# Kernel optimization log

Hardware: AMD Instinct MI355X
Metric: run time of the kernel (lower is better)

The kernel has to match this reference:

```python
import jax, jax.numpy as jnp
import numpy as np

OMEGA = 1.5

def _sine(x, W, b, omega=OMEGA):
    return jnp.sin(omega * (x @ W.T + b))

def setup_inputs() -> dict:
    key = jax.random.key(0)
    ks = jax.random.split(key, 17)
    I = J = K = 384
    mid, R = 256, 100
    s = 0.05  # small init scale, mimics uniform(-1/in, 1/in) style init
    return {
        "A_input": jax.random.normal(ks[0], (I, 1), jnp.float32),
        "B_input": jax.random.normal(ks[1], (J, 1), jnp.float32),
        "C_input": jax.random.normal(ks[2], (K, 1), jnp.float32),
        "A_W1": jax.random.normal(ks[3], (mid, 1), jnp.float32) * s,
        "A_b1": jax.random.normal(ks[4], (mid,), jnp.float32) * s,
        "A_W2": jax.random.normal(ks[5], (R, mid), jnp.float32) * s,
        "A_b2": jax.random.normal(ks[6], (R,), jnp.float32) * s,
        "B_W1": jax.random.normal(ks[7], (mid, 1), jnp.float32) * s,
        "B_b1": jax.random.normal(ks[8], (mid,), jnp.float32) * s,
        "B_W2": jax.random.normal(ks[9], (R, mid), jnp.float32) * s,
        "B_b2": jax.random.normal(ks[10], (R,), jnp.float32) * s,
        "C_W1": jax.random.normal(ks[11], (mid, 1), jnp.float32) * s,
        "C_b1": jax.random.normal(ks[12], (mid,), jnp.float32) * s,
        "C_W2": jax.random.normal(ks[13], (mid, mid), jnp.float32) * s,
        "C_b2": jax.random.normal(ks[14], (mid,), jnp.float32) * s,
        "C_W3": jax.random.normal(ks[15], (R, mid), jnp.float32) * s,
        "C_b3": jax.random.normal(ks[16], (R,), jnp.float32) * s,
    }

def reference(A_input, B_input, C_input,
              A_W1, A_b1, A_W2, A_b2,
              B_W1, B_b1, B_W2, B_b2,
              C_W1, C_b1, C_W2, C_b2, C_W3, C_b3):
    # Factor networks
    A = _sine(A_input, A_W1, A_b1) @ A_W2.T + A_b2                  # [I, R]
    B = _sine(B_input, B_W1, B_b1) @ B_W2.T + B_b2                  # [J, R]
    C = _sine(_sine(C_input, C_W1, C_b1), C_W2, C_b2) @ C_W3.T + C_b3  # [K, R]
    # The frozen core is super-diagonal (core[r,r,r]=1), so the permute/matmul
    # chain reduces exactly to the CP contraction sum_r A[i,r]*B[j,r]*C[k,r].
    return jnp.einsum('ir,jr,kr->ijk', A, B, C)  # [I, J, K]
```

## Files before the change

kernel.cpp:

```cpp
#include <hip/hip_runtime.h>
#include <hip/hip_bf16.h>

#define RR 100
#define MID 256
#define NN 384
#define KP 128

typedef __attribute__((ext_vector_type(8))) __bf16 bf16x8;
typedef __attribute__((ext_vector_type(4))) float floatx4;
typedef unsigned short ushort_t;

#define SW(row, ch) ((((row) << 7)) + ((((ch) ^ ((row) & 15))) << 3))

__device__ __forceinline__ ushort_t f2bf(float f) {
  __hip_bfloat16 h = __float2bfloat16(f);
  return __builtin_bit_cast(ushort_t, h);
}

__global__ __launch_bounds__(256) void factors_kernel(
    const float* __restrict__ xA, const float* __restrict__ xB,
    const float* __restrict__ xC,
    const float* __restrict__ AW1, const float* __restrict__ Ab1,
    const float* __restrict__ AW2, const float* __restrict__ Ab2,
    const float* __restrict__ BW1, const float* __restrict__ Bb1,
    const float* __restrict__ BW2, const float* __restrict__ Bb2,
    const float* __restrict__ CW1, const float* __restrict__ Cb1,
    const float* __restrict__ CW2, const float* __restrict__ Cb2,
    const float* __restrict__ CW3, const float* __restrict__ Cb3,
    float* __restrict__ Af, float* __restrict__ Bf,
    ushort_t* __restrict__ Cbf) {
  __shared__ float h[MID];
  __shared__ float h2[MID];
  const int i = blockIdx.x;
  const int net = blockIdx.y;
  const int t = threadIdx.x;

  const float* x  = (net == 0) ? xA  : (net == 1) ? xB  : xC;
  const float* W1 = (net == 0) ? AW1 : (net == 1) ? BW1 : CW1;
  const float* b1 = (net == 0) ? Ab1 : (net == 1) ? Bb1 : Cb1;

  const float xv = x[i];
  h[t] = sinf(1.5f * (xv * W1[t] + b1[t]));
  __syncthreads();

  const float* hlast = h;
  if (net == 2) {
    float acc = Cb2[t];
    const float* __restrict__ w = &CW2[t * MID];
#pragma unroll 4
    for (int m = 0; m < MID; m += 4) {
      const float4 wv = *(const float4*)&w[m];
      const float4 hv = *(const float4*)&h[m];
      acc += hv.x * wv.x;
      acc += hv.y * wv.y;
      acc += hv.z * wv.z;
      acc += hv.w * wv.w;
    }
    h2[t] = sinf(1.5f * acc);
    __syncthreads();
    hlast = h2;
  }

  const float* W2 = (net == 0) ? AW2 : (net == 1) ? BW2 : CW3;
  const float* b2 = (net == 0) ? Ab2 : (net == 1) ? Bb2 : Cb3;

  if (t < KP) {
    float v = 0.0f;
    if (t < RR) {
      float acc = b2[t];
      const float* __restrict__ w = &W2[t * MID];
#pragma unroll 4
      for (int m = 0; m < MID; m += 4) {
        const float4 wv = *(const float4*)&w[m];
        const float4 hv = *(const float4*)&hlast[m];
        acc += hv.x * wv.x;
        acc += hv.y * wv.y;
        acc += hv.z * wv.z;
        acc += hv.w * wv.w;
      }
      v = acc;
    }
    if (net == 0)      Af[i * KP + t] = v;
    else if (net == 1) Bf[i * KP + t] = v;
    else               Cbf[i * KP + t] = f2bf(v);
  }
}

__global__ __launch_bounds__(256, 3) void cp_mfma(
    const float* __restrict__ Af, const float* __restrict__ Bf,
    const ushort_t* __restrict__ Cbf, float* __restrict__ out) {
  __shared__ ushort_t Wt[64 * KP];
  __shared__ ushort_t Ct[128 * KP];

  const int bid = blockIdx.x;
  const int swz = (bid & 7) * 288 + (bid >> 3);
  const int i   = swz / 6;
  const int j0  = (swz % 6) * 64;
  const int t   = threadIdx.x;

  {
    const int jx = t >> 2;
    const int q  = t & 3;
    const float* __restrict__ arow = Af + (size_t)i * KP + q * 32;
    const float* __restrict__ brow = Bf + (size_t)(j0 + jx) * KP + q * 32;
#pragma unroll
    for (int c = 0; c < 4; ++c) {
      const float4 a0 = *(const float4*)(arow + c * 8);
      const float4 a1 = *(const float4*)(arow + c * 8 + 4);
      const float4 b0 = *(const float4*)(brow + c * 8);
      const float4 b1 = *(const float4*)(brow + c * 8 + 4);
      uint4 wv;
      wv.x = (unsigned)f2bf(a0.x * b0.x) | ((unsigned)f2bf(a0.y * b0.y) << 16);
      wv.y = (unsigned)f2bf(a0.z * b0.z) | ((unsigned)f2bf(a0.w * b0.w) << 16);
      wv.z = (unsigned)f2bf(a1.x * b1.x) | ((unsigned)f2bf(a1.y * b1.y) << 16);
      wv.w = (unsigned)f2bf(a1.z * b1.z) | ((unsigned)f2bf(a1.w * b1.w) << 16);
      *(uint4*)&Wt[SW(jx, q * 4 + c)] = wv;
    }
  }

  const int lane = t & 63;
  const int w    = t >> 6;
  const int m16  = lane & 15;
  const int g    = lane >> 4;
  const int jrow = j0 + w * 16 + m16;
  const size_t obase = (size_t)i * NN * NN + (size_t)jrow * NN;

  const int crow = t >> 4;
  const int cch  = t & 15;
  const ushort_t* __restrict__ csrc = Cbf + (size_t)crow * KP + cch * 8;
  const int swbase = SW(crow, cch);

  uint4 ca[8], cb[8];
#pragma unroll
  for (int it = 0; it < 8; ++it)
    ca[it] = *(const uint4*)(csrc + (size_t)(16 * it) * KP);

#define DS_WRITE(BUF)                                                        \
  {                                                                          \
    _Pragma("unroll") for (int it = 0; it < 8; ++it) {                       \
      *(uint4*)&Ct[SW(crow + 16 * it, cch)] = BUF[it];                       \
    }                                                                        \
  }

#define PREFETCH(BUF, KT)                                                    \
  {                                                                          \
    _Pragma("unroll") for (int it = 0; it < 8; ++it) {                       \
      BUF[it] = *(const uint4*)(csrc + (size_t)((KT) * 128 + 16 * it) * KP); \
    }                                                                        \
  }

#define COMPUTE_STORE(KT)                                                    \
  {                                                                          \
    const int kb = (KT) * 128 + g * 4;                                       \
    _Pragma("unroll") for (int kf = 0; kf < 8; ++kf) {                       \
      floatx4 a = (floatx4)0.0f;                                             \
      _Pragma("unroll") for (int ks = 0; ks < 4; ++ks) {                     \
        const bf16x8 cf =                                                    \
            *(const bf16x8*)&Ct[SW(kf * 16 + m16, ks * 4 + g)];              \
        a = __builtin_amdgcn_mfma_f32_16x16x32_bf16(cf, wfr[ks], a, 0, 0, 0);\
      }                                                                      \
      *(floatx4*)&out[obase + kb + kf * 16] = a;                             \
    }                                                                        \
  }

  DS_WRITE(ca);
  PREFETCH(cb, 1);
  __syncthreads();

  bf16x8 wfr[4];
#pragma unroll
  for (int ks = 0; ks < 4; ++ks)
    wfr[ks] = *(const bf16x8*)&Wt[SW(w * 16 + m16, ks * 4 + g)];

  COMPUTE_STORE(0);

  __syncthreads();
  DS_WRITE(cb);
  PREFETCH(ca, 2);
  __syncthreads();
  COMPUTE_STORE(1);

  __syncthreads();
  DS_WRITE(ca);
  __syncthreads();
  COMPUTE_STORE(2);

#undef DS_WRITE
#undef PREFETCH
#undef COMPUTE_STORE
}

extern "C" void kernel_launch(void* const* d_in, const int* in_sizes, int n_in,
                              void* d_out, int out_size, void* d_ws, size_t ws_size,
                              hipStream_t stream) {
  const float* A_input = (const float*)d_in[0];
  const float* B_input = (const float*)d_in[1];
  const float* C_input = (const float*)d_in[2];
  const float* A_W1 = (const float*)d_in[3];
  const float* A_b1 = (const float*)d_in[4];
  const float* A_W2 = (const float*)d_in[5];
  const float* A_b2 = (const float*)d_in[6];
  const float* B_W1 = (const float*)d_in[7];
  const float* B_b1 = (const float*)d_in[8];
  const float* B_W2 = (const float*)d_in[9];
  const float* B_b2 = (const float*)d_in[10];
  const float* C_W1 = (const float*)d_in[11];
  const float* C_b1 = (const float*)d_in[12];
  const float* C_W2 = (const float*)d_in[13];
  const float* C_b2 = (const float*)d_in[14];
  const float* C_W3 = (const float*)d_in[15];
  const float* C_b3 = (const float*)d_in[16];

  float* Af = (float*)d_ws;
  float* Bf = Af + NN * KP;
  ushort_t* Cbf = (ushort_t*)(Bf + NN * KP);

  dim3 fgrid(NN, 3);
  factors_kernel<<<fgrid, 256, 0, stream>>>(
      A_input, B_input, C_input,
      A_W1, A_b1, A_W2, A_b2,
      B_W1, B_b1, B_W2, B_b2,
      C_W1, C_b1, C_W2, C_b2, C_W3, C_b3,
      Af, Bf, Cbf);

  cp_mfma<<<dim3((NN / 64) * NN), 256, 0, stream>>>(Af, Bf, Cbf, (float*)d_out);
}
```

Measured before the change: 345.6 us.

## Retile wave work to 64j x 32k fragments and drop register prefetch

Each wave now computes all 64 j-rows for a 32-wide slice of k per tile, holding the W fragments for all j in registers and loading only two C fragments per k-step. This cuts LDS reads of C per MFMA. The register double-buffered global prefetch of C is replaced by direct global-to-LDS staging, which reduces register use but exposes global load latency between tiles.

```diff
diff --git a/kernel.cpp b/kernel.cpp
--- a/kernel.cpp
+++ b/kernel.cpp
@@ -122,71 +122,69 @@
   const int w    = t >> 6;
   const int m16  = lane & 15;
   const int g    = lane >> 4;
-  const int jrow = j0 + w * 16 + m16;
-  const size_t obase = (size_t)i * NN * NN + (size_t)jrow * NN;
+
+  size_t jbase[4];
+#pragma unroll
+  for (int jf = 0; jf < 4; ++jf)
+    jbase[jf] = (size_t)i * NN * NN + (size_t)(j0 + jf * 16 + m16) * NN;
 
   const int crow = t >> 4;
   const int cch  = t & 15;
   const ushort_t* __restrict__ csrc = Cbf + (size_t)crow * KP + cch * 8;
-  const int swbase = SW(crow, cch);
-
-  uint4 ca[8], cb[8];
-#pragma unroll
-  for (int it = 0; it < 8; ++it)
-    ca[it] = *(const uint4*)(csrc + (size_t)(16 * it) * KP);
-
-#define DS_WRITE(BUF)                                                        \
+
+#define STAGE(KT)                                                            \
   {                                                                          \
     _Pragma("unroll") for (int it = 0; it < 8; ++it) {                       \
-      *(uint4*)&Ct[SW(crow + 16 * it, cch)] = BUF[it];                       \
-    }                                                                        \
-  }
-
-#define PREFETCH(BUF, KT)                                                    \
-  {                                                                          \
-    _Pragma("unroll") for (int it = 0; it < 8; ++it) {                       \
-      BUF[it] = *(const uint4*)(csrc + (size_t)((KT) * 128 + 16 * it) * KP); \
+      *(uint4*)&Ct[SW(crow + 16 * it, cch)] =                                \
+          *(const uint4*)(csrc + (size_t)((KT) * 128 + 16 * it) * KP);       \
     }                                                                        \
   }
 
 #define COMPUTE_STORE(KT)                                                    \
   {                                                                          \
-    const int kb = (KT) * 128 + g * 4;                                       \
-    _Pragma("unroll") for (int kf = 0; kf < 8; ++kf) {                       \
-      floatx4 a = (floatx4)0.0f;                                             \
-      _Pragma("unroll") for (int ks = 0; ks < 4; ++ks) {                     \
-        const bf16x8 cf =                                                    \
-            *(const bf16x8*)&Ct[SW(kf * 16 + m16, ks * 4 + g)];              \
-        a = __builtin_amdgcn_mfma_f32_16x16x32_bf16(cf, wfr[ks], a, 0, 0, 0);\
-      }                                                                      \
-      *(floatx4*)&out[obase + kb + kf * 16] = a;                             \
+    floatx4 acc[4][2];                                                       \
+    _Pragma("unroll") for (int jf = 0; jf < 4; ++jf)                         \
+        _Pragma("unroll") for (int kf = 0; kf < 2; ++kf)                     \
+            acc[jf][kf] = (floatx4)0.0f;                                     \
+    _Pragma("unroll") for (int ks = 0; ks < 4; ++ks) {                       \
+      bf16x8 cf[2];                                                          \
+      _Pragma("unroll") for (int kf = 0; kf < 2; ++kf)                       \
+          cf[kf] = *(const bf16x8*)&Ct[SW(w * 32 + kf * 16 + m16,            \
+                                          ks * 4 + g)];                      \
+      _Pragma("unroll") for (int jf = 0; jf < 4; ++jf)                       \
+          _Pragma("unroll") for (int kf = 0; kf < 2; ++kf)                   \
+              acc[jf][kf] = __builtin_amdgcn_mfma_f32_16x16x32_bf16(         \
+                  cf[kf], wfr[jf][ks], acc[jf][kf], 0, 0, 0);                \
     }                                                                        \
-  }
-
-  DS_WRITE(ca);
-  PREFETCH(cb, 1);
-  __syncthreads();
-
-  bf16x8 wfr[4];
-#pragma unroll
-  for (int ks = 0; ks < 4; ++ks)
-    wfr[ks] = *(const bf16x8*)&Wt[SW(w * 16 + m16, ks * 4 + g)];
+    const int kb = (KT) * 128 + w * 32 + g * 4;                              \
+    _Pragma("unroll") for (int jf = 0; jf < 4; ++jf)                         \
+        _Pragma("unroll") for (int kf = 0; kf < 2; ++kf)                     \
+            *(floatx4*)&out[jbase[jf] + kb + kf * 16] = acc[jf][kf];         \
+  }
+
+  STAGE(0);
+  __syncthreads();
+
+  bf16x8 wfr[4][4];
+#pragma unroll
+  for (int jf = 0; jf < 4; ++jf)
+#pragma unroll
+    for (int ks = 0; ks < 4; ++ks)
+      wfr[jf][ks] = *(const bf16x8*)&Wt[SW(jf * 16 + m16, ks * 4 + g)];
 
   COMPUTE_STORE(0);
 
   __syncthreads();
-  DS_WRITE(cb);
-  PREFETCH(ca, 2);
+  STAGE(1);
   __syncthreads();
   COMPUTE_STORE(1);
 
   __syncthreads();
-  DS_WRITE(ca);
+  STAGE(2);
   __syncthreads();
   COMPUTE_STORE(2);
 
-#undef DS_WRITE
-#undef PREFETCH
+#undef STAGE
 #undef COMPUTE_STORE
 }
 
```

New measurement: 290.9 us. -15.8%, faster.
